# Kernel tuning notes

Hardware: AMD Instinct MI355X
Metric: run time of the kernel (lower is better)

## Reference

```python
import jax, jax.numpy as jnp
import numpy as np

NEG_INF = -1.0e9  # masked_fill value used by the torch module
LN_EPS = 1e-6


def setup_inputs() -> dict:
    key = jax.random.key(0)
    ks = jax.random.split(key, 10)
    B, S, D = 4, 1024, 1024
    H, DK, DV = 16, 64, 64
    q = jax.random.normal(ks[0], (B, S, D), dtype=jnp.float32)
    k = jax.random.normal(ks[1], (B, S, D), dtype=jnp.float32)
    v = jax.random.normal(ks[2], (B, S, D), dtype=jnp.float32)
    mask = jax.random.randint(ks[3], (B, S, S), 0, 2, dtype=jnp.int32)
    sc = 1.0 / np.sqrt(D)
    wq = jax.random.normal(ks[4], (H, D, DK), dtype=jnp.float32) * sc  # per-head W_qs stacked
    wk = jax.random.normal(ks[5], (H, D, DK), dtype=jnp.float32) * sc
    wv = jax.random.normal(ks[6], (H, D, DV), dtype=jnp.float32) * sc
    fc_w = jax.random.normal(ks[7], (D, H * DV), dtype=jnp.float32) * (1.0 / np.sqrt(H * DV))  # torch Linear weight [out,in]
    ln_g = jnp.ones((D,), dtype=jnp.float32)
    ln_b = jnp.zeros((D,), dtype=jnp.float32)
    return {"q": q, "k": k, "v": v, "mask": mask, "wq": wq, "wk": wk,
            "wv": wv, "fc_w": fc_w, "ln_g": ln_g, "ln_b": ln_b}


def reference(q, k, v, mask, wq, wk, wv, fc_w, ln_g, ln_b):
    # Batched equivalent of the per-head Python loop (dropout in eval mode = identity).
    B, S, D = q.shape
    H, _, DK = wq.shape
    DV = wv.shape[-1]
    temperature = jnp.asarray(DK, q.dtype) ** 0.5
    residual = q
    qh = jnp.einsum('bqd,hdk->bhqk', q, wq)   # [B,H,Q,DK]
    kh = jnp.einsum('bsd,hdk->bhsk', k, wk)   # [B,H,K,DK]
    vh = jnp.einsum('bsd,hdv->bhsv', v, wv)   # [B,H,K,DV]
    attn = jnp.einsum('bhqe,bhke->bhqk', qh / temperature, kh)  # [B,H,Q,K]
    attn = jnp.where(mask[:, None, :, :] == 0, jnp.asarray(NEG_INF, attn.dtype), attn)
    attn = jax.nn.softmax(attn, axis=-1)
    heads = jnp.einsum('bhqk,bhkv->bhqv', attn, vh)             # [B,H,Q,DV]
    # concat heads along feature dim in head order (matches torch.cat of the loop outputs)
    concat = jnp.transpose(heads, (0, 2, 1, 3)).reshape(B, S, H * DV)
    out = concat @ fc_w.T                                        # fc, no bias
    out = out + residual
    mu = jnp.mean(out, axis=-1, keepdims=True)
    var = jnp.mean(jnp.square(out - mu), axis=-1, keepdims=True)
    out = (out - mu) / jnp.sqrt(var + LN_EPS) * ln_g + ln_b
    return out
```

## Files before the change

### kernel.cpp

```cpp
#include <hip/hip_runtime.h>
#include <hip/hip_bf16.h>

typedef __bf16 bf16x8 __attribute__((ext_vector_type(8)));
typedef __bf16 bf16x4 __attribute__((ext_vector_type(4)));
typedef __bf16 bf16x2 __attribute__((ext_vector_type(2)));
typedef float f32x4 __attribute__((ext_vector_type(4)));
typedef unsigned int u32x2 __attribute__((ext_vector_type(2)));

#define MFMA16(a, b, c) __builtin_amdgcn_mfma_f32_16x16x32_bf16(a, b, c, 0, 0, 0)

static constexpr int M_ = 4096;

__device__ __forceinline__ void gload_lds16(const void* g, void* l) {
  __builtin_amdgcn_global_load_lds((const __attribute__((address_space(1))) void*)g,
                                   (__attribute__((address_space(3))) void*)l, 16, 0, 0);
}

__device__ __forceinline__ float exp2_hw(float x) {
  float r;
  asm("v_exp_f32 %0, %1" : "=v"(r) : "v"(x));
  return r;
}

__device__ __forceinline__ bf16x8 cvt8(float4 x, float4 y) {
  bf16x8 o;
  o[0] = (__bf16)x.x; o[1] = (__bf16)x.y; o[2] = (__bf16)x.z; o[3] = (__bf16)x.w;
  o[4] = (__bf16)y.x; o[5] = (__bf16)y.y; o[6] = (__bf16)y.z; o[7] = (__bf16)y.w;
  return o;
}

#define SWZ(rowv, c16) (((rowv) * 64) + (((c16) ^ ((rowv) & 7)) * 8))

__global__ __launch_bounds__(256) void cvt3(const float* __restrict__ q,
                                            const float* __restrict__ k,
                                            const float* __restrict__ v,
                                            __bf16* __restrict__ out) {
  const float* src = blockIdx.y == 0 ? q : (blockIdx.y == 1 ? k : v);
  __bf16* dst = out + (size_t)blockIdx.y * 4194304;
  int i = blockIdx.x * 256 + threadIdx.x;
  const float4* p = (const float4*)src + (size_t)i * 2;
  float4 a = p[0], b = p[1];
  *((bf16x8*)dst + i) = cvt8(a, b);
}

__global__ __launch_bounds__(256) void prep(const float* __restrict__ fc_w,
                                            const float* __restrict__ wq,
                                            const float* __restrict__ wk,
                                            const float* __restrict__ wv,
                                            const int* __restrict__ mask,
                                            __bf16* __restrict__ WFC,
                                            __bf16* __restrict__ W3T,
                                            unsigned long long* __restrict__ bits) {
  __shared__ float tile[64][65];
  int bx = blockIdx.x;
  const int t = threadIdx.x;

  if (bx < 512) {
    int i = bx * 256 + t;
    const float4* p = (const float4*)fc_w + (size_t)i * 2;
    float4 a = p[0], b = p[1];
    *((bf16x8*)WFC + i) = cvt8(a, b);
    return;
  }
  bx -= 512;
  if (bx < 768) {
    const int z = bx >> 8, rem = bx & 255;
    const float* w = z == 0 ? wq : (z == 1 ? wk : wv);
    const float scale = z == 0 ? 0.125f * 1.4426950408889634f : 1.0f;
    __bf16* o = W3T + (size_t)z * 1048576;
    const int h = rem & 15, d0 = (rem >> 4) * 64;
    const int r = t >> 2, c0 = (t & 3) * 16;
    const float4* s4 = (const float4*)(w + ((size_t)h * 1024 + d0 + r) * 64 + c0);
#pragma unroll
    for (int j = 0; j < 4; ++j) {
      float4 vv = s4[j];
      tile[r][c0 + 4 * j + 0] = vv.x; tile[r][c0 + 4 * j + 1] = vv.y;
      tile[r][c0 + 4 * j + 2] = vv.z; tile[r][c0 + 4 * j + 3] = vv.w;
    }
    __syncthreads();
    __bf16* dst = o + ((size_t)(h * 64 + r)) * 1024 + d0 + c0;
    bf16x8 o0, o1;
#pragma unroll
    for (int j = 0; j < 8; ++j) o0[j] = (__bf16)(tile[c0 + j][r] * scale);
#pragma unroll
    for (int j = 0; j < 8; ++j) o1[j] = (__bf16)(tile[c0 + 8 + j][r] * scale);
    *(bf16x8*)dst = o0;
    *(bf16x8*)(dst + 8) = o1;
    return;
  }
  bx -= 768;
  {
    const int wid = bx * 4 + (t >> 6);
    const int lane = t & 63;
#pragma unroll
    for (int i = 0; i < 16; ++i) {
      int widx = wid * 16 + i;
      int qrow = widx & 1023;
      int bkt = widx >> 10;
      int b = bkt >> 4, kt = bkt & 15;
      int mval = mask[((size_t)b * 1024 + qrow) * 1024 + kt * 64 + lane];
      unsigned long long bal = __ballot(mval != 0);
      if (lane == 0) bits[widx] = bal;
    }
  }
}

__global__ __launch_bounds__(256) void gemm_qkv(const __bf16* __restrict__ Abase,
                                                const __bf16* __restrict__ Btbase,
                                                __bf16* __restrict__ HEADS) {
  __shared__ __bf16 SMEM[16384];
  const int L = blockIdx.x;
  const int wl = (L & 7) * 96 + (L >> 3);
  const int bn = wl & 7;
  const int bmz = wl >> 3;
  const int bm = bmz & 31, z = bmz >> 5;
  const __bf16* A = Abase + (size_t)z * 4194304;
  const __bf16* Bt = Btbase + (size_t)z * 1048576;
  const int tid = threadIdx.x, lane = tid & 63;
  const int w = tid >> 6;
  const int wr = (w >> 1) * 64, wc = (w & 1) * 64;
  const int lr = lane & 15, lh = lane >> 4;

  const int o0 = tid * 16;
  const int row0 = o0 >> 6, cb = o0 & 63;
  const char* apA0 = (const char*)A + ((size_t)(bm * 128 + row0) * 1024) * 2 + cb;
  const char* apA1 = apA0 + 64 * 2048;
  const char* apB0 = (const char*)Bt + ((size_t)(bn * 128 + row0) * 1024) * 2 + cb;
  const char* apB1 = apB0 + 64 * 2048;
  char* smem = (char*)SMEM;

#define QSTAGE(buf)                                         \
  do {                                                      \
    char* dd = smem + (buf) * 16384;                        \
    gload_lds16(apA0, dd + o0);                             \
    gload_lds16(apA1, dd + 4096 + o0);                      \
    gload_lds16(apB0, dd + 8192 + o0);                      \
    gload_lds16(apB1, dd + 12288 + o0);                     \
    apA0 += 64; apA1 += 64; apB0 += 64; apB1 += 64;         \
  } while (0)

  f32x4 acc[4][4];
#pragma unroll
  for (int m = 0; m < 4; ++m)
#pragma unroll
    for (int n = 0; n < 4; ++n) {
      f32x4 zz = {0.f, 0.f, 0.f, 0.f};
      acc[m][n] = zz;
    }

  QSTAGE(0);
  __syncthreads();

  for (int kt = 0; kt < 32; ++kt) {
    const int cur = kt & 1;
    if (kt < 31) QSTAGE(cur ^ 1);
    const int abase = cur * 8192;
    bf16x8 af[4], bfr[4];
#pragma unroll
    for (int m = 0; m < 4; ++m)
      af[m] = *(const bf16x8*)&SMEM[abase + (wr + m * 16 + lr) * 32 + lh * 8];
#pragma unroll
    for (int n = 0; n < 4; ++n)
      bfr[n] = *(const bf16x8*)&SMEM[abase + 4096 + (wc + n * 16 + lr) * 32 + lh * 8];
    __builtin_amdgcn_s_setprio(1);
#pragma unroll
    for (int m = 0; m < 4; ++m)
#pragma unroll
      for (int n = 0; n < 4; ++n) acc[m][n] = MFMA16(af[m], bfr[n], acc[m][n]);
    __builtin_amdgcn_s_setprio(0);
    __syncthreads();
  }
#undef QSTAGE

  if (z == 2) {
    const int hl = w & 1;
    const size_t vtbase = 2ull * 4194304;
    const size_t bb = (size_t)(bm >> 3) * 16 + bn * 2;
    const int kkbase = (bm & 7) * 128;
#pragma unroll
    for (int p = 0; p < 2; ++p) {
      if (hl == p) {
#pragma unroll
        for (int m = 0; m < 4; ++m)
#pragma unroll
          for (int n = 0; n < 4; ++n) {
            const int dk = n * 16 + lr;
            const int s = wr + m * 16 + lh * 4;
            bf16x4 pv;
#pragma unroll
            for (int j = 0; j < 4; ++j) pv[j] = (__bf16)acc[m][n][j];
            *(bf16x4*)&SMEM[dk * 132 + s] = pv;
          }
      }
      __syncthreads();
      {
        const int dk = tid >> 2, sc = tid & 3;
        const __bf16* srcp = &SMEM[dk * 132 + sc * 32];
        __bf16* dstp = HEADS + vtbase + ((bb + p) * 64 + dk) * 1024 + kkbase + sc * 32;
#pragma unroll
        for (int u = 0; u < 8; ++u) *(bf16x4*)(dstp + u * 4) = *(const bf16x4*)(srcp + u * 4);
      }
      __syncthreads();
    }
    return;
  }

#pragma unroll
  for (int p = 0; p < 2; ++p) {
    if ((w >> 1) == p) {
#pragma unroll
      for (int m = 0; m < 4; ++m)
#pragma unroll
        for (int n = 0; n < 4; ++n)
#pragma unroll
          for (int reg = 0; reg < 4; ++reg)
            SMEM[(m * 16 + lh * 4 + reg) * 132 + wc + n * 16 + lr] = (__bf16)acc[m][n][reg];
    }
    __syncthreads();
    {
      const int rowl = tid >> 2, c0 = (tid & 3) * 32;
      const int row = bm * 128 + p * 64 + rowl;
      const int b = row >> 10, s = row & 1023;
      const int h = bn * 2 + (c0 >> 6), dk0 = c0 & 63;
      __bf16* dst = HEADS + (size_t)z * 4194304 + (((size_t)b * 16 + h) * 1024 + s) * 64 + dk0;
      const __bf16* srcp = &SMEM[rowl * 132 + c0];
#pragma unroll
      for (int u = 0; u < 8; ++u) *(bf16x4*)(dst + u * 4) = *(const bf16x4*)(srcp + u * 4);
    }
    __syncthreads();
  }
}

__global__ __launch_bounds__(256) void gemm_fc64(const __bf16* __restrict__ A,
                                                 const __bf16* __restrict__ Bt,
                                                 float* __restrict__ O,
                                                 const float* __restrict__ resid) {
  __shared__ __bf16 SMEM[12288];
  const int L = blockIdx.x;
  const int wl = (L & 7) * 64 + (L >> 3);
  const int bn = wl & 7, bm = wl >> 3;
  const int tid = threadIdx.x, lane = tid & 63;
  const int w = tid >> 6;
  const int wc = w * 32;
  const int lr = lane & 15, lh = lane >> 4;

  const int o0 = tid * 16;
  const int row0 = o0 >> 6, cb = o0 & 63;
  const char* apA = (const char*)A + ((size_t)(bm * 64 + row0) * 1024) * 2 + cb;
  const char* apB0 = (const char*)Bt + ((size_t)(bn * 128 + row0) * 1024) * 2 + cb;
  const char* apB1 = apB0 + 64 * 2048;
  char* smem = (char*)SMEM;

#define FSTAGE(buf)                                         \
  do {                                                      \
    gload_lds16(apA, smem + (buf) * 4096 + o0);             \
    char* dd = smem + 8192 + (buf) * 8192;                  \
    gload_lds16(apB0, dd + o0);                             \
    gload_lds16(apB1, dd + 4096 + o0);                      \
    apA += 64; apB0 += 64; apB1 += 64;                      \
  } while (0)

  f32x4 acc[4][2];
#pragma unroll
  for (int m = 0; m < 4; ++m)
#pragma unroll
    for (int n = 0; n < 2; ++n) {
      f32x4 z = {0.f, 0.f, 0.f, 0.f};
      acc[m][n] = z;
    }

  FSTAGE(0);
  __syncthreads();

  for (int kt = 0; kt < 32; ++kt) {
    const int cur = kt & 1;
    if (kt < 31) FSTAGE(cur ^ 1);
    const int ab = cur * 2048;
    const int bb = 4096 + cur * 4096;
    bf16x8 af[4], bfr[2];
#pragma unroll
    for (int m = 0; m < 4; ++m) af[m] = *(const bf16x8*)&SMEM[ab + (m * 16 + lr) * 32 + lh * 8];
#pragma unroll
    for (int n = 0; n < 2; ++n)
      bfr[n] = *(const bf16x8*)&SMEM[bb + (wc + n * 16 + lr) * 32 + lh * 8];
    __builtin_amdgcn_s_setprio(1);
#pragma unroll
    for (int m = 0; m < 4; ++m)
#pragma unroll
      for (int n = 0; n < 2; ++n) acc[m][n] = MFMA16(af[m], bfr[n], acc[m][n]);
    __builtin_amdgcn_s_setprio(0);
    __syncthreads();
  }
#undef FSTAGE

#pragma unroll
  for (int m = 0; m < 4; ++m)
#pragma unroll
    for (int n = 0; n < 2; ++n)
#pragma unroll
      for (int reg = 0; reg < 4; ++reg) {
        int row = bm * 64 + m * 16 + lh * 4 + reg;
        int col = bn * 128 + wc + n * 16 + lr;
        size_t idx = (size_t)row * 1024 + col;
        O[idx] = acc[m][n][reg] + resid[idx];
      }
}

__global__ __launch_bounds__(256, 4) void attn_kernel(const __bf16* __restrict__ HEADS,
                                                      const unsigned long long* __restrict__ m64,
                                                      __bf16* __restrict__ concat) {
  const __bf16* QH = HEADS;
  const __bf16* KH = HEADS + (size_t)M_ * 1024;
  const __bf16* VT = HEADS + (size_t)2 * M_ * 1024;
  __shared__ __bf16 Ks[2][2][32 * 64];
  __shared__ __bf16 Vs[2][2][64 * 32];
  __shared__ unsigned Psw[2][4][256];

  const int d = blockIdx.x;
  const int xcd = d & 7, j = d >> 3;
  const int grp = xcd * 8 + (j >> 4);
  const int qt = j & 15;
  const int h = grp & 15, b = grp >> 4;

  const int tid = threadIdx.x, lane = tid & 63, w = tid >> 6;
  const int lr = lane & 15, lh = lane >> 4;
  const size_t headoff = ((size_t)b * 16 + h) * 65536;
  const char* Kbase = (const char*)(KH + headoff);
  const char* Vbase = (const char*)(VT + headoff);

  const int krow = tid >> 3, kg = tid & 7;
  const int kgo = krow * 128 + ((kg ^ (krow & 7)) * 16);
  const int vrow = tid >> 2, vg = tid & 3;
  const int vgo = vrow * 2048 + ((vg ^ ((vrow >> 1) & 3)) * 16);
  const int ldsb = tid * 16;

  const char* kpA = Kbase + kgo;
  const char* kpB = Kbase + 65536 + kgo;
  const char* vpA = Vbase + vgo;
  const char* vpB = Vbase + 1024 + vgo;

#define STAGE(buf)                                          \
  do {                                                      \
    gload_lds16(kpA, (char*)Ks[buf][0] + ldsb);             \
    gload_lds16(kpB, (char*)Ks[buf][1] + ldsb);             \
    gload_lds16(vpA, (char*)Vs[buf][0] + ldsb);             \
    gload_lds16(vpB, (char*)Vs[buf][1] + ldsb);             \
    kpA += 4096; kpB += 4096; vpA += 64; vpB += 64;         \
  } while (0)

  const int qrow = qt * 64 + w * 16 + lr;
  bf16x8 qa[2];
  {
    const __bf16* qptr = QH + headoff + (size_t)qrow * 64 + lh * 8;
    qa[0] = *(const bf16x8*)qptr;
    qa[1] = *(const bf16x8*)(qptr + 32);
  }
  f32x4 oacc[4];
#pragma unroll
  for (int g = 0; g < 4; ++g) {
    f32x4 z = {0.f, 0.f, 0.f, 0.f};
    oacc[g] = z;
  }
  float lrun = 0.f;

  const unsigned long long* m64A = m64 + (size_t)b * 16384 + qrow;
  const unsigned long long* m64B = m64A + 8192;
  unsigned long long pairA = m64A[0], pairB = m64B[0];
  unsigned long long pairAn = 0, pairBn = 0;

  const int vcol = (lh ^ ((lr >> 1) & 3)) * 8;
  const int pread = lr * 32 + vcol;
  const int pG = (lr >> 1) & 3;
  int kread[2][2], vread[4];
#pragma unroll
  for (int n = 0; n < 2; ++n)
#pragma unroll
    for (int h2 = 0; h2 < 2; ++h2) kread[n][h2] = SWZ(n * 16 + lr, h2 * 4 + lh);
#pragma unroll
  for (int g = 0; g < 4; ++g) vread[g] = (g * 16 + lr) * 32 + vcol;

  STAGE(0);
  __syncthreads();

#pragma unroll 2
  for (int t = 0; t < 16; ++t) {
    const int cur = t & 1;
    if ((t & 1) == 0 && t < 14) {
      pairAn = m64A[((t >> 1) + 1) * 1024];
      pairBn = m64B[((t >> 1) + 1) * 1024];
    }
    const unsigned mwA = (t & 1) ? (unsigned)(pairA >> 32) : (unsigned)pairA;
    const unsigned mwB = (t & 1) ? (unsigned)(pairB >> 32) : (unsigned)pairB;
    if (t < 15) STAGE(cur ^ 1);

    f32x4 sA[2], sB[2];
#pragma unroll
    for (int n = 0; n < 2; ++n) {
      f32x4 z = {0.f, 0.f, 0.f, 0.f};
      sA[n] = z; sB[n] = z;
    }
    __builtin_amdgcn_s_setprio(1);
#pragma unroll
    for (int n = 0; n < 2; ++n)
#pragma unroll
      for (int h2 = 0; h2 < 2; ++h2) {
        bf16x8 kbA = *(const bf16x8*)&Ks[cur][0][kread[n][h2]];
        bf16x8 kbB = *(const bf16x8*)&Ks[cur][1][kread[n][h2]];
        sA[n] = MFMA16(kbA, qa[h2], sA[n]);
        sB[n] = MFMA16(kbB, qa[h2], sB[n]);
      }
    __builtin_amdgcn_s_setprio(0);

#pragma unroll
    for (int n = 0; n < 2; ++n)
#pragma unroll
      for (int r = 0; r < 4; ++r) {
        unsigned bit = (mwA >> (n * 16 + lh * 4 + r)) & 1u;
        float p = bit ? exp2_hw(sA[n][r]) : 0.0f;
        sA[n][r] = p;
        lrun += p;
      }
#pragma unroll
    for (int n = 0; n < 2; ++n)
#pragma unroll
      for (int r = 0; r < 4; ++r) {
        unsigned bit = (mwB >> (n * 16 + lh * 4 + r)) & 1u;
        float p = bit ? exp2_hw(sB[n][r]) : 0.0f;
        sB[n][r] = p;
        lrun += p;
      }

#pragma unroll
    for (int n = 0; n < 2; ++n) {
      bf16x2 p0, p1;
      p0[0] = (__bf16)sA[n][0]; p0[1] = (__bf16)sA[n][1];
      p1[0] = (__bf16)sA[n][2]; p1[1] = (__bf16)sA[n][3];
      int G = n * 2 + (lh >> 1);
      int addr = lr * 16 + ((G ^ pG) * 4) + (lh & 1) * 2;
      u32x2 wv;
      wv[0] = __builtin_bit_cast(unsigned, p0);
      wv[1] = __builtin_bit_cast(unsigned, p1);
      *(u32x2*)&Psw[0][w][addr] = wv;
    }
#pragma unroll
    for (int n = 0; n < 2; ++n) {
      bf16x2 p0, p1;
      p0[0] = (__bf16)sB[n][0]; p0[1] = (__bf16)sB[n][1];
      p1[0] = (__bf16)sB[n][2]; p1[1] = (__bf16)sB[n][3];
      int G = n * 2 + (lh >> 1);
      int addr = lr * 16 + ((G ^ pG) * 4) + (lh & 1) * 2;
      u32x2 wv;
      wv[0] = __builtin_bit_cast(unsigned, p0);
      wv[1] = __builtin_bit_cast(unsigned, p1);
      *(u32x2*)&Psw[1][w][addr] = wv;
    }
    bf16x8 paA = *(const bf16x8*)&((const __bf16*)Psw[0][w])[pread];
    bf16x8 paB = *(const bf16x8*)&((const __bf16*)Psw[1][w])[pread];

    __builtin_amdgcn_s_setprio(1);
#pragma unroll
    for (int g = 0; g < 4; ++g) {
      bf16x8 vbA = *(const bf16x8*)&Vs[cur][0][vread[g]];
      bf16x8 vbB = *(const bf16x8*)&Vs[cur][1][vread[g]];
      oacc[g] = MFMA16(paA, vbA, oacc[g]);
      oacc[g] = MFMA16(paB, vbB, oacc[g]);
    }
    __builtin_amdgcn_s_setprio(0);
    if (t & 1) { pairA = pairAn; pairB = pairBn; }
    __syncthreads();
  }
#undef STAGE

  lrun += __shfl_xor(lrun, 16, 64);
  lrun += __shfl_xor(lrun, 32, 64);
  const float linv = 1.0f / (lrun + 1e-30f);
  const int qg0 = qt * 64 + w * 16 + lh * 4;
#pragma unroll
  for (int r = 0; r < 4; ++r) {
    const float ir = __shfl(linv, (lane & 48) | (lh * 4 + r), 64);
#pragma unroll
    for (int g = 0; g < 4; ++g)
      concat[((size_t)b * 1024 + qg0 + r) * 1024 + h * 64 + g * 16 + lr] =
          (__bf16)(oacc[g][r] * ir);
  }
}

__global__ __launch_bounds__(256) void ln_kernel(const float* __restrict__ in,
                                                 const float* __restrict__ gam,
                                                 const float* __restrict__ bet,
                                                 float* __restrict__ out) {
  const int row = blockIdx.x, t = threadIdx.x;
  const float4* x4 = (const float4*)(in + (size_t)row * 1024);
  float4 v = x4[t];
  float s = v.x + v.y + v.z + v.w;
  float sq = v.x * v.x + v.y * v.y + v.z * v.z + v.w * v.w;
#pragma unroll
  for (int off = 1; off < 64; off <<= 1) {
    s += __shfl_xor(s, off, 64);
    sq += __shfl_xor(sq, off, 64);
  }
  __shared__ float red[8];
  const int w = t >> 6, lane = t & 63;
  if (lane == 0) { red[w] = s; red[4 + w] = sq; }
  __syncthreads();
  s = red[0] + red[1] + red[2] + red[3];
  sq = red[4] + red[5] + red[6] + red[7];
  const float mu = s * (1.0f / 1024.0f);
  const float var = sq * (1.0f / 1024.0f) - mu * mu;
  const float rstd = rsqrtf(var + 1e-6f);
  float4 g4 = ((const float4*)gam)[t];
  float4 b4 = ((const float4*)bet)[t];
  float4 o;
  o.x = (v.x - mu) * rstd * g4.x + b4.x;
  o.y = (v.y - mu) * rstd * g4.y + b4.y;
  o.z = (v.z - mu) * rstd * g4.z + b4.z;
  o.w = (v.w - mu) * rstd * g4.w + b4.w;
  ((float4*)(out + (size_t)row * 1024))[t] = o;
}

extern "C" void kernel_launch(void* const* d_in, const int* in_sizes, int n_in,
                              void* d_out, int out_size, void* d_ws, size_t ws_size,
                              hipStream_t stream) {
  (void)in_sizes; (void)n_in; (void)out_size; (void)ws_size;
  const float* q = (const float*)d_in[0];
  const float* k = (const float*)d_in[1];
  const float* v = (const float*)d_in[2];
  const int* mask = (const int*)d_in[3];
  const float* wq = (const float*)d_in[4];
  const float* wk = (const float*)d_in[5];
  const float* wv = (const float*)d_in[6];
  const float* fc_w = (const float*)d_in[7];
  const float* ln_g = (const float*)d_in[8];
  const float* ln_b = (const float*)d_in[9];
  float* out = (float*)d_out;

  __bf16* QKVBF = (__bf16*)d_ws;
  __bf16* W3T   = QKVBF + 3ull * 4194304;
  __bf16* WFC   = W3T + 3ull * 1048576;
  __bf16* HEADS = WFC + 1048576;
  __bf16* CONCAT = HEADS + 3ull * 4194304;
  float* OUT1 = (float*)(CONCAT + 4194304);
  unsigned long long* MASKB = (unsigned long long*)OUT1;

  cvt3<<<dim3(2048, 3), 256, 0, stream>>>(q, k, v, QKVBF);
  prep<<<2304, 256, 0, stream>>>(fc_w, wq, wk, wv, mask, WFC, W3T, MASKB);
  gemm_qkv<<<768, 256, 0, stream>>>(QKVBF, W3T, HEADS);
  attn_kernel<<<1024, 256, 0, stream>>>(HEADS, MASKB, CONCAT);
  gemm_fc64<<<512, 256, 0, stream>>>(CONCAT, WFC, OUT1, q);
  ln_kernel<<<4096, 256, 0, stream>>>(OUT1, ln_g, ln_b, out);
}
```

Baseline: 121.9 us.

## Fuse fp32-to-bf16 conversion of q/k/v into the QKV projection GEMM

Removes the separate cvt3 kernel that converted q, k, v to bf16 in workspace. The QKV GEMM now streams fp32 A tiles directly into LDS with an XOR swizzle and converts to bf16 while loading the MFMA fragments. This drops one kernel launch and a write/read round trip of the bf16 activations. In exchange, the GEMM reads twice as many A bytes, uses more LDS (48KB), and converts in the inner loop.

Result: faster. 115.3 us (-5.4%).

```diff
diff --git a/kernel.cpp b/kernel.cpp
--- a/kernel.cpp
+++ b/kernel.cpp
@@ -30,18 +30,6 @@
 }
 
 #define SWZ(rowv, c16) (((rowv) * 64) + (((c16) ^ ((rowv) & 7)) * 8))
-
-__global__ __launch_bounds__(256) void cvt3(const float* __restrict__ q,
-                                            const float* __restrict__ k,
-                                            const float* __restrict__ v,
-                                            __bf16* __restrict__ out) {
-  const float* src = blockIdx.y == 0 ? q : (blockIdx.y == 1 ? k : v);
-  __bf16* dst = out + (size_t)blockIdx.y * 4194304;
-  int i = blockIdx.x * 256 + threadIdx.x;
-  const float4* p = (const float4*)src + (size_t)i * 2;
-  float4 a = p[0], b = p[1];
-  *((bf16x8*)dst + i) = cvt8(a, b);
-}
 
 __global__ __launch_bounds__(256) void prep(const float* __restrict__ fc_w,
                                             const float* __restrict__ wq,
@@ -105,39 +93,49 @@
   }
 }
 
-__global__ __launch_bounds__(256) void gemm_qkv(const __bf16* __restrict__ Abase,
+__global__ __launch_bounds__(256) void gemm_qkv(const float* __restrict__ q,
+                                                const float* __restrict__ k,
+                                                const float* __restrict__ v,
                                                 const __bf16* __restrict__ Btbase,
                                                 __bf16* __restrict__ HEADS) {
-  __shared__ __bf16 SMEM[16384];
+  __shared__ __bf16 SMEM[24576];
   const int L = blockIdx.x;
   const int wl = (L & 7) * 96 + (L >> 3);
   const int bn = wl & 7;
   const int bmz = wl >> 3;
   const int bm = bmz & 31, z = bmz >> 5;
-  const __bf16* A = Abase + (size_t)z * 4194304;
+  const float* Af = z == 0 ? q : (z == 1 ? k : v);
   const __bf16* Bt = Btbase + (size_t)z * 1048576;
   const int tid = threadIdx.x, lane = tid & 63;
   const int w = tid >> 6;
   const int wr = (w >> 1) * 64, wc = (w & 1) * 64;
   const int lr = lane & 15, lh = lane >> 4;
-
-  const int o0 = tid * 16;
-  const int row0 = o0 >> 6, cb = o0 & 63;
-  const char* apA0 = (const char*)A + ((size_t)(bm * 128 + row0) * 1024) * 2 + cb;
-  const char* apA1 = apA0 + 64 * 2048;
-  const char* apB0 = (const char*)Bt + ((size_t)(bn * 128 + row0) * 1024) * 2 + cb;
-  const char* apB1 = apB0 + 64 * 2048;
+  const int t16 = tid * 16;
   char* smem = (char*)SMEM;
 
-#define QSTAGE(buf)                                         \
-  do {                                                      \
-    char* dd = smem + (buf) * 16384;                        \
-    gload_lds16(apA0, dd + o0);                             \
-    gload_lds16(apA1, dd + 4096 + o0);                      \
-    gload_lds16(apB0, dd + 8192 + o0);                      \
-    gload_lds16(apB1, dd + 12288 + o0);                     \
-    apA0 += 64; apA1 += 64; apB0 += 64; apB1 += 64;         \
+  const char* apA = (const char*)Af +
+                    ((size_t)(bm * 128 + (tid >> 3)) * 4096) +
+                    (((tid & 7) ^ ((tid >> 3) & 7)) * 16);
+  const char* apB = (const char*)Bt +
+                    ((size_t)(bn * 128 + (tid >> 2)) * 2048) +
+                    (((tid & 3) ^ ((tid >> 2) & 3)) * 16);
+
+#define QSTAGE(buf)                                              \
+  do {                                                           \
+    char* da = smem + (buf) * 16384;                             \
+    gload_lds16(apA, da + t16);                                  \
+    gload_lds16(apA + 131072, da + 4096 + t16);                  \
+    gload_lds16(apA + 262144, da + 8192 + t16);                  \
+    gload_lds16(apA + 393216, da + 12288 + t16);                 \
+    char* db = smem + 32768 + (buf) * 8192;                      \
+    gload_lds16(apB, db + t16);                                  \
+    gload_lds16(apB + 131072, db + 4096 + t16);                  \
+    apA += 128; apB += 64;                                       \
   } while (0)
+
+  const int aswz0 = (((2 * lh) ^ (lr & 7)) * 16);
+  const int aswz1 = (((2 * lh + 1) ^ (lr & 7)) * 16);
+  const int bswz = ((lh ^ (lr & 3)) * 16);
 
   f32x4 acc[4][4];
 #pragma unroll
@@ -154,14 +152,19 @@
   for (int kt = 0; kt < 32; ++kt) {
     const int cur = kt & 1;
     if (kt < 31) QSTAGE(cur ^ 1);
-    const int abase = cur * 8192;
+    const int abase = cur * 16384;
+    const int bbase = 32768 + cur * 8192;
     bf16x8 af[4], bfr[4];
 #pragma unroll
-    for (int m = 0; m < 4; ++m)
-      af[m] = *(const bf16x8*)&SMEM[abase + (wr + m * 16 + lr) * 32 + lh * 8];
+    for (int m = 0; m < 4; ++m) {
+      const char* ap = smem + abase + (wr + m * 16 + lr) * 128;
+      float4 f0 = *(const float4*)(ap + aswz0);
+      float4 f1 = *(const float4*)(ap + aswz1);
+      af[m] = cvt8(f0, f1);
+    }
 #pragma unroll
     for (int n = 0; n < 4; ++n)
-      bfr[n] = *(const bf16x8*)&SMEM[abase + 4096 + (wc + n * 16 + lr) * 32 + lh * 8];
+      bfr[n] = *(const bf16x8*)(smem + bbase + (wc + n * 16 + lr) * 64 + bswz);
     __builtin_amdgcn_s_setprio(1);
 #pragma unroll
     for (int m = 0; m < 4; ++m)
@@ -175,7 +178,7 @@
   if (z == 2) {
     const int hl = w & 1;
     const size_t vtbase = 2ull * 4194304;
-    const size_t bb = (size_t)(bm >> 3) * 16 + bn * 2;
+    const size_t bb2 = (size_t)(bm >> 3) * 16 + bn * 2;
     const int kkbase = (bm & 7) * 128;
 #pragma unroll
     for (int p = 0; p < 2; ++p) {
@@ -196,7 +199,7 @@
       {
         const int dk = tid >> 2, sc = tid & 3;
         const __bf16* srcp = &SMEM[dk * 132 + sc * 32];
-        __bf16* dstp = HEADS + vtbase + ((bb + p) * 64 + dk) * 1024 + kkbase + sc * 32;
+        __bf16* dstp = HEADS + vtbase + ((bb2 + p) * 64 + dk) * 1024 + kkbase + sc * 32;
 #pragma unroll
         for (int u = 0; u < 8; ++u) *(bf16x4*)(dstp + u * 4) = *(const bf16x4*)(srcp + u * 4);
       }
@@ -542,9 +545,8 @@
   float* OUT1 = (float*)(CONCAT + 4194304);
   unsigned long long* MASKB = (unsigned long long*)OUT1;
 
-  cvt3<<<dim3(2048, 3), 256, 0, stream>>>(q, k, v, QKVBF);
   prep<<<2304, 256, 0, stream>>>(fc_w, wq, wk, wv, mask, WFC, W3T, MASKB);
-  gemm_qkv<<<768, 256, 0, stream>>>(QKVBF, W3T, HEADS);
+  gemm_qkv<<<768, 256, 0, stream>>>(q, k, v, W3T, HEADS);
   attn_kernel<<<1024, 256, 0, stream>>>(HEADS, MASKB, CONCAT);
   gemm_fc64<<<512, 256, 0, stream>>>(CONCAT, WFC, OUT1, q);
   ln_kernel<<<4096, 256, 0, stream>>>(OUT1, ln_g, ln_b, out);
```
